# Optimization experiments

Measured on AMD Instinct MI355X. Metric: run time of the kernel, lower is better.

Reference implementation:

```python
import jax, jax.numpy as jnp
import numpy as np

B, T, V, H, E = 64, 64, 32000, 512, 256
EPS = 0.1
CLAMP_MIN = 1e-8


def setup_inputs() -> dict:
    key = jax.random.key(0)
    ks = jax.random.split(key, 7)
    s = 0.05  # small init scale to keep logits in a sane range
    return {
        "embedding": jax.random.normal(ks[0], (V, E), jnp.float32) * s,
        "w_ih": jax.random.normal(ks[1], (3 * H, E), jnp.float32) * s,
        "b_ih": jax.random.normal(ks[2], (3 * H,), jnp.float32) * s,
        "w_hh": jax.random.normal(ks[3], (3 * H, H), jnp.float32) * s,
        "b_hh": jax.random.normal(ks[4], (3 * H,), jnp.float32) * s,
        "w_out": jax.random.normal(ks[5], (V, H), jnp.float32) * s,
        "b_out": jax.random.normal(ks[6], (V,), jnp.float32) * s,
    }


def _gru_cell(x, h, w_ih, b_ih, w_hh, b_hh):
    # torch GRUCell: gates ordered (r, z, n)
    gi = x @ w_ih.T + b_ih          # [B, 3H]
    gh = h @ w_hh.T + b_hh          # [B, 3H]
    gi_r, gi_z, gi_n = jnp.split(gi, 3, axis=1)
    gh_r, gh_z, gh_n = jnp.split(gh, 3, axis=1)
    r = jax.nn.sigmoid(gi_r + gh_r)
    z = jax.nn.sigmoid(gi_z + gh_z)
    n = jnp.tanh(gi_n + r * gh_n)
    return (1.0 - z) * n + z * h


def reference(embedding, w_ih, b_ih, w_hh, b_hh, w_out, b_out):
    log_unif = -jnp.log(jnp.float32(V))

    def step(carry, key):
        hidden, inputs = carry
        hidden = _gru_cell(inputs, hidden, w_ih, b_ih, w_hh, b_hh)
        dist = jax.nn.log_softmax(hidden @ w_out.T + b_out, axis=-1)  # [B, V]
        dist_new = jax.lax.stop_gradient(dist)
        prob = jnp.exp(dist_new)
        prob_mean = prob.mean(0)  # [V]
        k_eps, k_gum = jax.random.split(key)
        # eps-sample: with prob EPS replace row with uniform log-prob
        draw = EPS >= jax.random.uniform(k_eps, (B,))
        dist_eps = jnp.where(draw[:, None], log_unif, dist_new)
        # Gumbel-max sampling
        u = jax.random.uniform(k_gum, (B, V), minval=1e-9, maxval=1.0)
        sampled = jnp.argmax(dist_eps - jnp.log(-jnp.log(u)), axis=1)  # [B]
        idx = sampled[:, None]
        logprob = jnp.take_along_axis(dist, idx, axis=1)[:, 0]
        onpolicy = jnp.clip(jnp.take_along_axis(prob, idx, axis=1)[:, 0], CLAMP_MIN, 1.0)
        offpolicy = jnp.clip(jnp.exp(jnp.take_along_axis(dist_eps, idx, axis=1)[:, 0]), CLAMP_MIN, 1.0)
        correction = onpolicy / offpolicy
        inputs_next = embedding[sampled]  # [B, E]
        return (hidden, inputs_next), (sampled, correction, logprob, dist, prob_mean)

    hidden0 = jnp.zeros((B, H), jnp.float32)
    inputs0 = jnp.broadcast_to(embedding[0], (B, E))  # embedding of zero token
    keys = jax.random.split(jax.random.key(1), T)
    _, (samples, corrections, logprobs, dists, probs) = jax.lax.scan(
        step, (hidden0, inputs0), keys)
    # scan stacks along time: transpose to batch-major like torch.cat(dim=1)
    return (samples.T,            # [B, T] int
            corrections.T,        # [B, T]
            logprobs.T,           # [B, T]
            dists.transpose(1, 0, 2),  # [B, T, V]
            probs)                # [T, V]
```

## Files before the change

kernel.cpp:

```cpp
#include <hip/hip_runtime.h>
#include <cstdint>
#include <cstddef>


#define JAX_PARTITIONABLE 1

#define Bn 64
#define Tn 64
#define Vn 32000
#define Hn 512
#define En 256

#define NSTRIP 500
#define SPAD   512

typedef unsigned short u16;
typedef __attribute__((ext_vector_type(8))) __bf16 bf16x8;
typedef __attribute__((ext_vector_type(4))) float f32x4;
typedef __attribute__((ext_vector_type(4))) uint32_t u32x4;

#define OUT_SAMP 0
#define OUT_CORR (Bn * Tn)
#define OUT_LOGP (2 * Bn * Tn)
#define OUT_DIST (3 * Bn * Tn)
#define OUT_PROB (3 * Bn * Tn + (size_t)Bn * Tn * Vn)

#define WS_HT0  0
#define WS_HT1  (WS_HT0 + Hn * Bn)
#define WS_RM   (WS_HT1 + Hn * Bn)
#define WS_RL   (WS_RM + Tn * Bn)
#define WS_SMP  (WS_RL + Tn * Bn)
#define WS_CNT  (WS_SMP + Bn)
#define WS_HS0  (WS_CNT + Bn)
#define WS_HS1  (WS_HS0 + Bn * Hn / 2)
#define WS_HS2  (WS_HS1 + Bn * Hn / 2)
#define WS_PM   (WS_HS2 + Bn * Hn / 2)
#define WS_PS   (WS_PM + Bn * SPAD)
#define WS_PBS  (WS_PS + Bn * SPAD)
#define WS_PBV  (WS_PBS + Bn * SPAD)
#define WS_PBZ  (WS_PBV + Bn * SPAD)

__device__ __forceinline__ void tf2x32(uint32_t k0, uint32_t k1,
                                       uint32_t x0, uint32_t x1,
                                       uint32_t& o0, uint32_t& o1) {
  uint32_t ks2 = k0 ^ k1 ^ 0x1BD11BDAu;
  x0 += k0; x1 += k1;
#define TFR(r) { x0 += x1; x1 = (x1 << r) | (x1 >> (32 - r)); x1 ^= x0; }
  TFR(13) TFR(15) TFR(26) TFR(6)  x0 += k1;  x1 += ks2 + 1u;
  TFR(17) TFR(29) TFR(16) TFR(24) x0 += ks2; x1 += k0 + 2u;
  TFR(13) TFR(15) TFR(26) TFR(6)  x0 += k0;  x1 += k1 + 3u;
  TFR(17) TFR(29) TFR(16) TFR(24) x0 += k1;  x1 += ks2 + 4u;
  TFR(13) TFR(15) TFR(26) TFR(6)  x0 += ks2; x1 += k0 + 5u;
#undef TFR
  o0 = x0; o1 = x1;
}

__device__ __forceinline__ uint32_t jax_bits32(uint32_t k0, uint32_t k1,
                                               uint32_t i, uint32_t total) {
#if JAX_PARTITIONABLE
  (void)total;
  uint32_t o0, o1; tf2x32(k0, k1, 0u, i, o0, o1); return o0 ^ o1;
#else
  uint32_t half = total >> 1;
  uint32_t o0, o1;
  if (i < half) { tf2x32(k0, k1, i, i + half, o0, o1); return o0; }
  tf2x32(k0, k1, i - half, i, o0, o1); return o1;
#endif
}

__device__ __forceinline__ void jax_splitkey(uint32_t k0, uint32_t k1,
                                             uint32_t idx, uint32_t num,
                                             uint32_t& s0, uint32_t& s1) {
#if JAX_PARTITIONABLE
  (void)num;
  tf2x32(k0, k1, 0u, idx, s0, s1);
#else
  uint32_t j0 = 2 * idx, j1 = 2 * idx + 1;
  uint32_t r0, r1;
  if (j0 < num) { tf2x32(k0, k1, j0, j0 + num, r0, r1); s0 = r0; }
  else          { tf2x32(k0, k1, j0 - num, j0, r0, r1); s0 = r1; }
  if (j1 < num) { tf2x32(k0, k1, j1, j1 + num, r0, r1); s1 = r0; }
  else          { tf2x32(k0, k1, j1 - num, j1, r0, r1); s1 = r1; }
#endif
}

__device__ __forceinline__ float bits_to_unit(uint32_t bits) {
  return __uint_as_float((bits >> 9) | 0x3F800000u) - 1.0f;
}

struct Limbs3 { uint32_t p0, p1, p2; };

__device__ __forceinline__ Limbs3 split3_pair(float xa, float xb) {
  const uint32_t a0 = __float_as_uint(xa) & 0xFFFF0000u;
  const float ar1 = xa - __uint_as_float(a0);
  const uint32_t a1 = __float_as_uint(ar1) & 0xFFFF0000u;
  const float ar2 = ar1 - __uint_as_float(a1);
  const uint32_t a2 = __float_as_uint(ar2) & 0xFFFF0000u;
  const uint32_t b0 = __float_as_uint(xb) & 0xFFFF0000u;
  const float br1 = xb - __uint_as_float(b0);
  const uint32_t b1 = __float_as_uint(br1) & 0xFFFF0000u;
  const float br2 = br1 - __uint_as_float(b1);
  const uint32_t b2 = __float_as_uint(br2) & 0xFFFF0000u;
  Limbs3 r;
  r.p0 = (a0 >> 16) | b0;
  r.p1 = (a1 >> 16) | b1;
  r.p2 = (a2 >> 16) | b2;
  return r;
}


__global__ void init_k(float* h0, int* sampled, int* cnt) {
  int i = blockIdx.x * 256 + threadIdx.x;
  if (i < Bn * Hn) h0[i] = 0.0f;
  if (i < Bn) { sampled[i] = 0; cnt[i] = 0; }
}

__global__ __launch_bounds__(256) void gru_fused(
    const float* __restrict__ emb,
    const float* __restrict__ w_ih, const float* __restrict__ b_ih,
    const float* __restrict__ w_hh, const float* __restrict__ b_hh,
    const float* __restrict__ hT_prev, float* __restrict__ hT_new,
    const int* __restrict__ sampled,
    u16* __restrict__ hs0, u16* __restrict__ hs1, u16* __restrict__ hs2) {
  const int tid = threadIdx.x;
  const int b = tid & 63;
  const int w = __builtin_amdgcn_readfirstlane(tid >> 6);
  const int q = w & 1;
  const int kh = w >> 1;
  const int j = blockIdx.x * 2 + q;

  __shared__ float Xs[En][64];
  {
    const int g = tid >> 6;
    const float* src = emb + (size_t)sampled[b] * En + g * 64;
#pragma unroll
    for (int kk = 0; kk < 64; kk += 4) {
      float4 v = *(const float4*)(src + kk);
      Xs[g * 64 + kk + 0][b] = v.x;
      Xs[g * 64 + kk + 1][b] = v.y;
      Xs[g * 64 + kk + 2][b] = v.z;
      Xs[g * 64 + kk + 3][b] = v.w;
    }
  }
  __syncthreads();

  float a_r = 0.f, a_z = 0.f, a_n = 0.f;
  float g_r = 0.f, g_z = 0.f, g_n = 0.f;

  {
    const float* wr = w_ih + (size_t)j * En;
    const float* wz = w_ih + (size_t)(Hn + j) * En;
    const float* wn = w_ih + (size_t)(2 * Hn + j) * En;
    const int kb = kh * 128;
#pragma unroll 8
    for (int k = kb; k < kb + 128; k++) {
      const float xv = Xs[k][b];
      a_r = fmaf(xv, wr[k], a_r);
      a_z = fmaf(xv, wz[k], a_z);
      a_n = fmaf(xv, wn[k], a_n);
    }
  }
  {
    const float* wr = w_hh + (size_t)j * Hn;
    const float* wz = w_hh + (size_t)(Hn + j) * Hn;
    const float* wn = w_hh + (size_t)(2 * Hn + j) * Hn;
    const int kb = kh * 256;
#pragma unroll 8
    for (int k = kb; k < kb + 256; k++) {
      const float hv = hT_prev[k * 64 + b];
      g_r = fmaf(hv, wr[k], g_r);
      g_z = fmaf(hv, wz[k], g_z);
      g_n = fmaf(hv, wn[k], g_n);
    }
  }

  __shared__ float red[6][2][64];
  if (kh == 1) {
    red[0][q][b] = a_r; red[1][q][b] = a_z; red[2][q][b] = a_n;
    red[3][q][b] = g_r; red[4][q][b] = g_z; red[5][q][b] = g_n;
  }
  __syncthreads();
  if (kh == 0) {
    a_r += red[0][q][b]; a_z += red[1][q][b]; a_n += red[2][q][b];
    g_r += red[3][q][b]; g_z += red[4][q][b]; g_n += red[5][q][b];
    const float gr = a_r + b_ih[j] + g_r + b_hh[j];
    const float gz = a_z + b_ih[Hn + j] + g_z + b_hh[Hn + j];
    const float r = 1.0f / (1.0f + expf(-gr));
    const float z = 1.0f / (1.0f + expf(-gz));
    const float ghn = g_n + b_hh[2 * Hn + j];
    const float n = tanhf(a_n + b_ih[2 * Hn + j] + r * ghn);
    const float hp = hT_prev[j * 64 + b];
    const float h = (1.0f - z) * n + z * hp;
    hT_new[j * 64 + b] = h;
    const uint32_t c0 = __float_as_uint(h) & 0xFFFF0000u;
    const float r1 = h - __uint_as_float(c0);
    const uint32_t c1 = __float_as_uint(r1) & 0xFFFF0000u;
    const float r2 = r1 - __uint_as_float(c1);
    const size_t ho = (size_t)b * Hn + j;
    hs0[ho] = (u16)(c0 >> 16);
    hs1[ho] = (u16)(c1 >> 16);
    hs2[ho] = (u16)(__float_as_uint(r2) >> 16);
  }
}

__global__ __launch_bounds__(256, 2) void logits_mfma(
    const u16* __restrict__ hs0, const u16* __restrict__ hs1,
    const u16* __restrict__ hs2,
    const float* __restrict__ w_out, const float* __restrict__ b_out,
    float* __restrict__ out_dist,
    float* __restrict__ pM, float* __restrict__ pS, float* __restrict__ pBS,
    int* __restrict__ pBV, float* __restrict__ pBZ,
    int* __restrict__ cnt, float* __restrict__ rmA, float* __restrict__ rlA,
    int* __restrict__ sampled, float* __restrict__ out, int t) {
  const int tid = threadIdx.x;
  const int w = tid >> 6;
  const int lane = tid & 63;
  const int wm = (w >> 1) * 32;
  const int wn = (w & 1) * 32;
  const int lr = lane & 15;
  const int lg = lane >> 4;
  const int v0 = blockIdx.x * 64;

  __shared__ int s_dr[64];
  __shared__ float ldsM[64][2], ldsS[64][2], ldsBS[64][2], ldsBZ[64][2];
  __shared__ int ldsBV[64][2];
  __shared__ int s_tk;

  uint32_t kt0, kt1, kg0, kg1;
  jax_splitkey(0u, 1u, (uint32_t)t, (uint32_t)Tn, kt0, kt1);
  jax_splitkey(kt0, kt1, 1u, 2u, kg0, kg1);
  if (tid < 64) {
    uint32_t ke0, ke1;
    jax_splitkey(kt0, kt1, 0u, 2u, ke0, ke1);
    const uint32_t eb = jax_bits32(ke0, ke1, (uint32_t)tid, (uint32_t)Bn);
    s_dr[tid] = (0.1f >= bits_to_unit(eb)) ? 1 : 0;
  }
  __syncthreads();

  f32x4 acc[2][2] = {};

#pragma unroll 2
  for (int k0 = 0; k0 < Hn; k0 += 32) {
    bf16x8 a0[2], a1[2], a2[2];
#pragma unroll
    for (int mi = 0; mi < 2; mi++) {
      const size_t off = (size_t)(wm + mi * 16 + lr) * Hn + k0 + lg * 8;
      a0[mi] = *reinterpret_cast<const bf16x8*>(hs0 + off);
      a1[mi] = *reinterpret_cast<const bf16x8*>(hs1 + off);
      a2[mi] = *reinterpret_cast<const bf16x8*>(hs2 + off);
    }
    bf16x8 bb0[2], bb1[2], bb2[2];
#pragma unroll
    for (int ni = 0; ni < 2; ni++) {
      const float* src = w_out + (size_t)(v0 + wn + ni * 16 + lr) * Hn + k0 + lg * 8;
      const float4 x0 = *(const float4*)(src);
      const float4 x1 = *(const float4*)(src + 4);
      u32x4 q0, q1, q2;
      const Limbs3 l0 = split3_pair(x0.x, x0.y);
      const Limbs3 l1 = split3_pair(x0.z, x0.w);
      const Limbs3 l2 = split3_pair(x1.x, x1.y);
      const Limbs3 l3 = split3_pair(x1.z, x1.w);
      q0[0] = l0.p0; q1[0] = l0.p1; q2[0] = l0.p2;
      q0[1] = l1.p0; q1[1] = l1.p1; q2[1] = l1.p2;
      q0[2] = l2.p0; q1[2] = l2.p1; q2[2] = l2.p2;
      q0[3] = l3.p0; q1[3] = l3.p1; q2[3] = l3.p2;
      bb0[ni] = __builtin_bit_cast(bf16x8, q0);
      bb1[ni] = __builtin_bit_cast(bf16x8, q1);
      bb2[ni] = __builtin_bit_cast(bf16x8, q2);
    }
#pragma unroll
    for (int mi = 0; mi < 2; mi++)
#pragma unroll
      for (int ni = 0; ni < 2; ni++) {
        f32x4 c = acc[mi][ni];
        c = __builtin_amdgcn_mfma_f32_16x16x32_bf16(a0[mi], bb0[ni], c, 0, 0, 0);
        c = __builtin_amdgcn_mfma_f32_16x16x32_bf16(a0[mi], bb1[ni], c, 0, 0, 0);
        c = __builtin_amdgcn_mfma_f32_16x16x32_bf16(a1[mi], bb0[ni], c, 0, 0, 0);
        c = __builtin_amdgcn_mfma_f32_16x16x32_bf16(a1[mi], bb1[ni], c, 0, 0, 0);
        c = __builtin_amdgcn_mfma_f32_16x16x32_bf16(a0[mi], bb2[ni], c, 0, 0, 0);
        c = __builtin_amdgcn_mfma_f32_16x16x32_bf16(a2[mi], bb0[ni], c, 0, 0, 0);
        acc[mi][ni] = c;
      }
  }

  float bias[2];
#pragma unroll
  for (int ni = 0; ni < 2; ni++) bias[ni] = b_out[v0 + wn + ni * 16 + lr];
#pragma unroll
  for (int mi = 0; mi < 2; mi++)
#pragma unroll
    for (int ni = 0; ni < 2; ni++)
#pragma unroll
      for (int r = 0; r < 4; r++) {
        acc[mi][ni][r] += bias[ni];
        const int brow = wm + mi * 16 + lg * 4 + r;
        out_dist[(size_t)(brow * Tn + t) * Vn + v0 + wn + ni * 16 + lr] =
            acc[mi][ni][r];
      }

  const float LU = -logf((float)Vn);
#pragma unroll
  for (int mi = 0; mi < 2; mi++) {
#pragma unroll
    for (int r = 0; r < 4; r++) {
      const int brow = wm + mi * 16 + lg * 4 + r;
      const int dr = s_dr[brow];
      const int vA = v0 + wn + lr, vB = vA + 16;
      const float zA = acc[mi][0][r], zB = acc[mi][1][r];
      float mz = fmaxf(zA, zB);
#pragma unroll
      for (int off = 1; off < 16; off <<= 1) mz = fmaxf(mz, __shfl_xor(mz, off, 64));
      float sz = expf(zA - mz) + expf(zB - mz);
#pragma unroll
      for (int off = 1; off < 16; off <<= 1) sz += __shfl_xor(sz, off, 64);
      const uint32_t bA = jax_bits32(kg0, kg1, (uint32_t)(brow * Vn + vA), 0u);
      const uint32_t bB = jax_bits32(kg0, kg1, (uint32_t)(brow * Vn + vB), 0u);
      const float uA = fmaxf(1e-9f, bits_to_unit(bA) + 1e-9f);
      const float uB = fmaxf(1e-9f, bits_to_unit(bB) + 1e-9f);
      const float glA = logf(-logf(uA));
      const float glB = logf(-logf(uB));
      const float sA = (dr ? LU : zA) - glA;
      const float sB = (dr ? LU : zB) - glB;
      float bs; int bv; float bz;
      if (sB > sA) { bs = sB; bv = vB; bz = zB; }
      else         { bs = sA; bv = vA; bz = zA; }
#pragma unroll
      for (int off = 1; off < 16; off <<= 1) {
        const float so = __shfl_xor(bs, off, 64);
        const int vo = __shfl_xor(bv, off, 64);
        const float zo = __shfl_xor(bz, off, 64);
        if (so > bs || (so == bs && vo < bv)) { bs = so; bv = vo; bz = zo; }
      }
      if (lr == 0) {
        ldsM[brow][w & 1] = mz; ldsS[brow][w & 1] = sz;
        ldsBS[brow][w & 1] = bs; ldsBV[brow][w & 1] = bv; ldsBZ[brow][w & 1] = bz;
      }
    }
  }
  __syncthreads();
  if (tid < 64) {
    const float m0 = ldsM[tid][0], m1 = ldsM[tid][1];
    const float mm = fmaxf(m0, m1);
    const float ss = ldsS[tid][0] * expf(m0 - mm) + ldsS[tid][1] * expf(m1 - mm);
    float bs = ldsBS[tid][0]; int bv = ldsBV[tid][0]; float bz = ldsBZ[tid][0];
    if (ldsBS[tid][1] > bs || (ldsBS[tid][1] == bs && ldsBV[tid][1] < bv)) {
      bs = ldsBS[tid][1]; bv = ldsBV[tid][1]; bz = ldsBZ[tid][1];
    }
    const int o = tid * SPAD + blockIdx.x;
    pM[o] = mm; pS[o] = ss; pBS[o] = bs; pBV[o] = bv; pBZ[o] = bz;
  }
  __syncthreads();

  if (tid == 0) {
    __threadfence();
    s_tk = __hip_atomic_fetch_add(&cnt[t], 1, __ATOMIC_ACQ_REL,
                                  __HIP_MEMORY_SCOPE_AGENT);
  }
  __syncthreads();
  const int ticket = s_tk;
  if (ticket >= NSTRIP - 8 && ticket < NSTRIP) {
    while (__hip_atomic_load(&cnt[t], __ATOMIC_ACQUIRE,
                             __HIP_MEMORY_SCOPE_AGENT) < NSTRIP) {
      __builtin_amdgcn_s_sleep(8);
    }
    const int base = (ticket - (NSTRIP - 8)) * 8;
    const int g = tid >> 5, l32 = tid & 31;
    const int row = base + g;
    float m = -INFINITY, ssum = 0.f;
    float bs = -INFINITY; int bv = Vn; float bz = 0.f;
    for (int s = l32; s < NSTRIP; s += 32) {
      const int o = row * SPAD + s;
      const float m2 = pM[o], s2 = pS[o];
      const float mn = fmaxf(m, m2);
      ssum = ssum * expf(m - mn) + s2 * expf(m2 - mn);
      m = mn;
      const float b2 = pBS[o]; const int v2 = pBV[o];
      if (b2 > bs || (b2 == bs && v2 < bv)) { bs = b2; bv = v2; bz = pBZ[o]; }
    }
#pragma unroll
    for (int off = 16; off >= 1; off >>= 1) {
      const float mo = __shfl_xor(m, off, 64);
      const float so = __shfl_xor(ssum, off, 64);
      const float mn = fmaxf(m, mo);
      ssum = ssum * expf(m - mn) + so * expf(mo - mn);
      m = mn;
      const float bo = __shfl_xor(bs, off, 64);
      const int vo = __shfl_xor(bv, off, 64);
      const float zo = __shfl_xor(bz, off, 64);
      if (bo > bs || (bo == bs && vo < bv)) { bs = bo; bv = vo; bz = zo; }
    }
    if (l32 == 0) {
      const float l = logf(ssum);
      rmA[t * Bn + row] = m;
      rlA[t * Bn + row] = l;
      sampled[row] = bv;
      out[OUT_SAMP + row * Tn + t] = (float)bv;
      const float d = (bz - m) - l;
      out[OUT_LOGP + row * Tn + t] = d;
      uint32_t ke0, ke1;
      jax_splitkey(kt0, kt1, 0u, 2u, ke0, ke1);
      const int dr =
          (0.1f >= bits_to_unit(jax_bits32(ke0, ke1, (uint32_t)row, (uint32_t)Bn)))
              ? 1 : 0;
      const float onp = fminf(fmaxf(expf(d), 1e-8f), 1.0f);
      const float offp = fminf(fmaxf(expf(dr ? LU : d), 1e-8f), 1.0f);
      out[OUT_CORR + row * Tn + t] = onp / offp;
    }
  }
}

__global__ void norm_all_k(float* __restrict__ out_dist,
                           float* __restrict__ probs,
                           const float* __restrict__ rmA,
                           const float* __restrict__ rlA) {
  const int blk = blockIdx.x;
  const int t = blk / 250;
  const int c = blk % 250;
  const int tid = threadIdx.x;
  const int v = c * 128 + (tid & 127);
  const int half = tid >> 7;
  __shared__ float sm[64], sl[64];
  if (tid < 64) { sm[tid] = rmA[t * Bn + tid]; sl[tid] = rlA[t * Bn + tid]; }
  __syncthreads();
  float s = 0.f;
  for (int i = 0; i < 32; i++) {
    const int b = half * 32 + i;
    float* p = out_dist + (size_t)(b * Tn + t) * Vn + v;
    const float d = (*p - sm[b]) - sl[b];
    *p = d;
    s += expf(d);
  }
  __shared__ float red[256];
  red[tid] = s; __syncthreads();
  if (half == 0)
    probs[(size_t)t * Vn + v] = (red[tid] + red[tid + 128]) * 0.015625f;
}

extern "C" void kernel_launch(void* const* d_in, const int* in_sizes, int n_in,
                              void* d_out, int out_size, void* d_ws, size_t ws_size,
                              hipStream_t stream) {
  const float* emb   = (const float*)d_in[0];
  const float* w_ih  = (const float*)d_in[1];
  const float* b_ih  = (const float*)d_in[2];
  const float* w_hh  = (const float*)d_in[3];
  const float* b_hh  = (const float*)d_in[4];
  const float* w_out = (const float*)d_in[5];
  const float* b_out = (const float*)d_in[6];
  float* out = (float*)d_out;
  float* ws  = (float*)d_ws;

  float* hT[2] = { ws + WS_HT0, ws + WS_HT1 };
  float* rmA  = ws + WS_RM;
  float* rlA  = ws + WS_RL;
  int*   smp  = (int*)(ws + WS_SMP);
  int*   cnt  = (int*)(ws + WS_CNT);
  u16*   hs0  = (u16*)(ws + WS_HS0);
  u16*   hs1  = (u16*)(ws + WS_HS1);
  u16*   hs2  = (u16*)(ws + WS_HS2);
  float* pM   = ws + WS_PM;
  float* pS   = ws + WS_PS;
  float* pBS  = ws + WS_PBS;
  int*   pBV  = (int*)(ws + WS_PBV);
  float* pBZ  = ws + WS_PBZ;

  init_k<<<(Bn * Hn + 255) / 256, 256, 0, stream>>>(hT[0], smp, cnt);

  for (int t = 0; t < Tn; t++) {
    float* hp = hT[t & 1];
    float* hn = hT[(t + 1) & 1];
    gru_fused<<<Hn / 2, 256, 0, stream>>>(emb, w_ih, b_ih, w_hh, b_hh,
                                          hp, hn, smp, hs0, hs1, hs2);
    logits_mfma<<<NSTRIP, 256, 0, stream>>>(hs0, hs1, hs2, w_out, b_out,
                                            out + OUT_DIST, pM, pS, pBS, pBV, pBZ,
                                            cnt, rmA, rlA, smp, out, t);
  }
  norm_all_k<<<Tn * 250, 256, 0, stream>>>(out + OUT_DIST, out + OUT_PROB,
                                           rmA, rlA);
}
```

Measured before the change: 8.088 ms.

## Fuse GRU, logits and normalization into one persistent kernel with grid barriers

Replaces the per-timestep pair of kernel launches and the final normalization pass with a single persistent kernel of 250 blocks that loops over time and synchronizes through a global atomic grid barrier. The GRU cell moves onto MFMA using a 3-limb bf16 split, computed by 32 of the blocks. Logits stay in registers across the barrier, so normalized log-probs and the per-token probability mean are written once instead of being re-read and rewritten by a separate pass. This removes about 128 launches and one full pass over the large dist tensor. In exchange it depends on all 250 blocks being co-resident to avoid deadlock, pays for grid-wide barriers each step, and serializes the GRU work onto a subset of blocks.

Result: slower. 27.99 ms (+246.1%).

```diff
diff --git a/kernel.cpp b/kernel.cpp
--- a/kernel.cpp
+++ b/kernel.cpp
@@ -10,9 +10,8 @@
 #define Vn 32000
 #define Hn 512
 #define En 256
-
+#define NBLK 250
 #define NSTRIP 500
-#define SPAD   512
 
 typedef unsigned short u16;
 typedef __attribute__((ext_vector_type(8))) __bf16 bf16x8;
@@ -25,20 +24,14 @@
 #define OUT_DIST (3 * Bn * Tn)
 #define OUT_PROB (3 * Bn * Tn + (size_t)Bn * Tn * Vn)
 
-#define WS_HT0  0
-#define WS_HT1  (WS_HT0 + Hn * Bn)
-#define WS_RM   (WS_HT1 + Hn * Bn)
-#define WS_RL   (WS_RM + Tn * Bn)
-#define WS_SMP  (WS_RL + Tn * Bn)
-#define WS_CNT  (WS_SMP + Bn)
-#define WS_HS0  (WS_CNT + Bn)
-#define WS_HS1  (WS_HS0 + Bn * Hn / 2)
-#define WS_HS2  (WS_HS1 + Bn * Hn / 2)
-#define WS_PM   (WS_HS2 + Bn * Hn / 2)
-#define WS_PS   (WS_PM + Bn * SPAD)
-#define WS_PBS  (WS_PS + Bn * SPAD)
-#define WS_PBV  (WS_PBS + Bn * SPAD)
-#define WS_PBZ  (WS_PBV + Bn * SPAD)
+#define WS_HT  0
+#define WS_HS  (2 * Hn * 64)
+#define WS_PM  (WS_HS + 3 * Bn * Hn)
+#define WS_PS  (WS_PM + NSTRIP * Bn)
+#define WS_PBS (WS_PS + NSTRIP * Bn)
+#define WS_PBV (WS_PBS + NSTRIP * Bn)
+#define WS_PBZ (WS_PBV + NSTRIP * Bn)
+#define WS_BAR (WS_PBZ + NSTRIP * Bn)
 
 __device__ __forceinline__ void tf2x32(uint32_t k0, uint32_t k1,
                                        uint32_t x0, uint32_t x1,
@@ -56,32 +49,14 @@
 }
 
 __device__ __forceinline__ uint32_t jax_bits32(uint32_t k0, uint32_t k1,
-                                               uint32_t i, uint32_t total) {
-#if JAX_PARTITIONABLE
-  (void)total;
+                                               uint32_t i) {
   uint32_t o0, o1; tf2x32(k0, k1, 0u, i, o0, o1); return o0 ^ o1;
-#else
-  uint32_t half = total >> 1;
-  uint32_t o0, o1;
-  if (i < half) { tf2x32(k0, k1, i, i + half, o0, o1); return o0; }
-  tf2x32(k0, k1, i - half, i, o0, o1); return o1;
-#endif
 }
 
 __device__ __forceinline__ void jax_splitkey(uint32_t k0, uint32_t k1,
-                                             uint32_t idx, uint32_t num,
+                                             uint32_t idx,
                                              uint32_t& s0, uint32_t& s1) {
-#if JAX_PARTITIONABLE
-  (void)num;
   tf2x32(k0, k1, 0u, idx, s0, s1);
-#else
-  uint32_t j0 = 2 * idx, j1 = 2 * idx + 1;
-  uint32_t r0, r1;
-  if (j0 < num) { tf2x32(k0, k1, j0, j0 + num, r0, r1); s0 = r0; }
-  else          { tf2x32(k0, k1, j0 - num, j0, r0, r1); s0 = r1; }
-  if (j1 < num) { tf2x32(k0, k1, j1, j1 + num, r0, r1); s1 = r0; }
-  else          { tf2x32(k0, k1, j1 - num, j1, r0, r1); s1 = r1; }
-#endif
 }
 
 __device__ __forceinline__ float bits_to_unit(uint32_t bits) {
@@ -108,110 +83,67 @@
   return r;
 }
 
-
-__global__ void init_k(float* h0, int* sampled, int* cnt) {
-  int i = blockIdx.x * 256 + threadIdx.x;
-  if (i < Bn * Hn) h0[i] = 0.0f;
-  if (i < Bn) { sampled[i] = 0; cnt[i] = 0; }
-}
-
-__global__ __launch_bounds__(256) void gru_fused(
+__device__ __forceinline__ void split3_frag(const float4& x0, const float4& x1,
+                                            uint32_t msk,
+                                            bf16x8& f0, bf16x8& f1, bf16x8& f2) {
+  u32x4 q0, q1, q2;
+  const Limbs3 l0 = split3_pair(x0.x, x0.y);
+  const Limbs3 l1 = split3_pair(x0.z, x0.w);
+  const Limbs3 l2 = split3_pair(x1.x, x1.y);
+  const Limbs3 l3 = split3_pair(x1.z, x1.w);
+  q0[0] = l0.p0 & msk; q1[0] = l0.p1 & msk; q2[0] = l0.p2 & msk;
+  q0[1] = l1.p0 & msk; q1[1] = l1.p1 & msk; q2[1] = l1.p2 & msk;
+  q0[2] = l2.p0 & msk; q1[2] = l2.p1 & msk; q2[2] = l2.p2 & msk;
+  q0[3] = l3.p0 & msk; q1[3] = l3.p1 & msk; q2[3] = l3.p2 & msk;
+  f0 = __builtin_bit_cast(bf16x8, q0);
+  f1 = __builtin_bit_cast(bf16x8, q1);
+  f2 = __builtin_bit_cast(bf16x8, q2);
+}
+
+__device__ __forceinline__ f32x4 mfma6(const bf16x8& a0, const bf16x8& a1,
+                                       const bf16x8& a2, const bf16x8& b0,
+                                       const bf16x8& b1, const bf16x8& b2,
+                                       f32x4 c) {
+  c = __builtin_amdgcn_mfma_f32_16x16x32_bf16(a0, b0, c, 0, 0, 0);
+  c = __builtin_amdgcn_mfma_f32_16x16x32_bf16(a0, b1, c, 0, 0, 0);
+  c = __builtin_amdgcn_mfma_f32_16x16x32_bf16(a1, b0, c, 0, 0, 0);
+  c = __builtin_amdgcn_mfma_f32_16x16x32_bf16(a1, b1, c, 0, 0, 0);
+  c = __builtin_amdgcn_mfma_f32_16x16x32_bf16(a0, b2, c, 0, 0, 0);
+  c = __builtin_amdgcn_mfma_f32_16x16x32_bf16(a2, b0, c, 0, 0, 0);
+  return c;
+}
+
+__device__ __forceinline__ void gridbar(int* bar, int target) {
+  __syncthreads();
+  if (threadIdx.x == 0) {
+    __threadfence();
+    __hip_atomic_fetch_add(bar, 1, __ATOMIC_ACQ_REL, __HIP_MEMORY_SCOPE_AGENT);
+    while (__hip_atomic_load(bar, __ATOMIC_ACQUIRE,
+                             __HIP_MEMORY_SCOPE_AGENT) < target) {
+      __builtin_amdgcn_s_sleep(1);
+    }
+  }
+  __syncthreads();
+  __threadfence();
+}
+
+__global__ void init_k(float* hT, uint32_t* hsw, int* bar) {
+  const int i = blockIdx.x * 256 + threadIdx.x;
+  if (i < 2 * Hn * 64) hT[i] = 0.0f;
+  if (i < 3 * Bn * Hn) hsw[i] = 0u;
+  if (i == 0) *bar = 0;
+}
+
+__global__ __launch_bounds__(256, 2) void mega(
     const float* __restrict__ emb,
     const float* __restrict__ w_ih, const float* __restrict__ b_ih,
     const float* __restrict__ w_hh, const float* __restrict__ b_hh,
-    const float* __restrict__ hT_prev, float* __restrict__ hT_new,
-    const int* __restrict__ sampled,
-    u16* __restrict__ hs0, u16* __restrict__ hs1, u16* __restrict__ hs2) {
-  const int tid = threadIdx.x;
-  const int b = tid & 63;
-  const int w = __builtin_amdgcn_readfirstlane(tid >> 6);
-  const int q = w & 1;
-  const int kh = w >> 1;
-  const int j = blockIdx.x * 2 + q;
-
-  __shared__ float Xs[En][64];
-  {
-    const int g = tid >> 6;
-    const float* src = emb + (size_t)sampled[b] * En + g * 64;
-#pragma unroll
-    for (int kk = 0; kk < 64; kk += 4) {
-      float4 v = *(const float4*)(src + kk);
-      Xs[g * 64 + kk + 0][b] = v.x;
-      Xs[g * 64 + kk + 1][b] = v.y;
-      Xs[g * 64 + kk + 2][b] = v.z;
-      Xs[g * 64 + kk + 3][b] = v.w;
-    }
-  }
-  __syncthreads();
-
-  float a_r = 0.f, a_z = 0.f, a_n = 0.f;
-  float g_r = 0.f, g_z = 0.f, g_n = 0.f;
-
-  {
-    const float* wr = w_ih + (size_t)j * En;
-    const float* wz = w_ih + (size_t)(Hn + j) * En;
-    const float* wn = w_ih + (size_t)(2 * Hn + j) * En;
-    const int kb = kh * 128;
-#pragma unroll 8
-    for (int k = kb; k < kb + 128; k++) {
-      const float xv = Xs[k][b];
-      a_r = fmaf(xv, wr[k], a_r);
-      a_z = fmaf(xv, wz[k], a_z);
-      a_n = fmaf(xv, wn[k], a_n);
-    }
-  }
-  {
-    const float* wr = w_hh + (size_t)j * Hn;
-    const float* wz = w_hh + (size_t)(Hn + j) * Hn;
-    const float* wn = w_hh + (size_t)(2 * Hn + j) * Hn;
-    const int kb = kh * 256;
-#pragma unroll 8
-    for (int k = kb; k < kb + 256; k++) {
-      const float hv = hT_prev[k * 64 + b];
-      g_r = fmaf(hv, wr[k], g_r);
-      g_z = fmaf(hv, wz[k], g_z);
-      g_n = fmaf(hv, wn[k], g_n);
-    }
-  }
-
-  __shared__ float red[6][2][64];
-  if (kh == 1) {
-    red[0][q][b] = a_r; red[1][q][b] = a_z; red[2][q][b] = a_n;
-    red[3][q][b] = g_r; red[4][q][b] = g_z; red[5][q][b] = g_n;
-  }
-  __syncthreads();
-  if (kh == 0) {
-    a_r += red[0][q][b]; a_z += red[1][q][b]; a_n += red[2][q][b];
-    g_r += red[3][q][b]; g_z += red[4][q][b]; g_n += red[5][q][b];
-    const float gr = a_r + b_ih[j] + g_r + b_hh[j];
-    const float gz = a_z + b_ih[Hn + j] + g_z + b_hh[Hn + j];
-    const float r = 1.0f / (1.0f + expf(-gr));
-    const float z = 1.0f / (1.0f + expf(-gz));
-    const float ghn = g_n + b_hh[2 * Hn + j];
-    const float n = tanhf(a_n + b_ih[2 * Hn + j] + r * ghn);
-    const float hp = hT_prev[j * 64 + b];
-    const float h = (1.0f - z) * n + z * hp;
-    hT_new[j * 64 + b] = h;
-    const uint32_t c0 = __float_as_uint(h) & 0xFFFF0000u;
-    const float r1 = h - __uint_as_float(c0);
-    const uint32_t c1 = __float_as_uint(r1) & 0xFFFF0000u;
-    const float r2 = r1 - __uint_as_float(c1);
-    const size_t ho = (size_t)b * Hn + j;
-    hs0[ho] = (u16)(c0 >> 16);
-    hs1[ho] = (u16)(c1 >> 16);
-    hs2[ho] = (u16)(__float_as_uint(r2) >> 16);
-  }
-}
-
-__global__ __launch_bounds__(256, 2) void logits_mfma(
-    const u16* __restrict__ hs0, const u16* __restrict__ hs1,
-    const u16* __restrict__ hs2,
     const float* __restrict__ w_out, const float* __restrict__ b_out,
-    float* __restrict__ out_dist,
+    float* __restrict__ out,
+    float* __restrict__ hT, u16* __restrict__ hs,
     float* __restrict__ pM, float* __restrict__ pS, float* __restrict__ pBS,
-    int* __restrict__ pBV, float* __restrict__ pBZ,
-    int* __restrict__ cnt, float* __restrict__ rmA, float* __restrict__ rlA,
-    int* __restrict__ sampled, float* __restrict__ out, int t) {
+    int* __restrict__ pBV, float* __restrict__ pBZ, int* __restrict__ bar) {
+  const int blk = blockIdx.x;
   const int tid = threadIdx.x;
   const int w = tid >> 6;
   const int lane = tid & 63;
@@ -219,221 +151,337 @@
   const int wn = (w & 1) * 32;
   const int lr = lane & 15;
   const int lg = lane >> 4;
-  const int v0 = blockIdx.x * 64;
-
+  const bool isGru = (blk < 32);
+  const float LU = -logf((float)Vn);
+
+  __shared__ float s_m[64], s_l[64];
+  __shared__ int s_smp[64];
   __shared__ int s_dr[64];
   __shared__ float ldsM[64][2], ldsS[64][2], ldsBS[64][2], ldsBZ[64][2];
   __shared__ int ldsBV[64][2];
-  __shared__ int s_tk;
-
-  uint32_t kt0, kt1, kg0, kg1;
-  jax_splitkey(0u, 1u, (uint32_t)t, (uint32_t)Tn, kt0, kt1);
-  jax_splitkey(kt0, kt1, 1u, 2u, kg0, kg1);
-  if (tid < 64) {
-    uint32_t ke0, ke1;
-    jax_splitkey(kt0, kt1, 0u, 2u, ke0, ke1);
-    const uint32_t eb = jax_bits32(ke0, ke1, (uint32_t)tid, (uint32_t)Bn);
-    s_dr[tid] = (0.1f >= bits_to_unit(eb)) ? 1 : 0;
-  }
+  __shared__ float Gs[64][66];
+  __shared__ float pc[2][64];
+
+  if (tid < 64) s_smp[tid] = 0;
   __syncthreads();
 
-  f32x4 acc[2][2] = {};
-
-#pragma unroll 2
-  for (int k0 = 0; k0 < Hn; k0 += 32) {
-    bf16x8 a0[2], a1[2], a2[2];
-#pragma unroll
-    for (int mi = 0; mi < 2; mi++) {
-      const size_t off = (size_t)(wm + mi * 16 + lr) * Hn + k0 + lg * 8;
-      a0[mi] = *reinterpret_cast<const bf16x8*>(hs0 + off);
-      a1[mi] = *reinterpret_cast<const bf16x8*>(hs1 + off);
-      a2[mi] = *reinterpret_cast<const bf16x8*>(hs2 + off);
-    }
-    bf16x8 bb0[2], bb1[2], bb2[2];
+  const float* gruIh[2];
+  const float* gruHh[2];
+  float gruBias[2];
+  uint32_t gruMih[2], gruMhh[2];
+  if (isGru) {
 #pragma unroll
     for (int ni = 0; ni < 2; ni++) {
-      const float* src = w_out + (size_t)(v0 + wn + ni * 16 + lr) * Hn + k0 + lg * 8;
-      const float4 x0 = *(const float4*)(src);
-      const float4 x1 = *(const float4*)(src + 4);
-      u32x4 q0, q1, q2;
-      const Limbs3 l0 = split3_pair(x0.x, x0.y);
-      const Limbs3 l1 = split3_pair(x0.z, x0.w);
-      const Limbs3 l2 = split3_pair(x1.x, x1.y);
-      const Limbs3 l3 = split3_pair(x1.z, x1.w);
-      q0[0] = l0.p0; q1[0] = l0.p1; q2[0] = l0.p2;
-      q0[1] = l1.p0; q1[1] = l1.p1; q2[1] = l1.p2;
-      q0[2] = l2.p0; q1[2] = l2.p1; q2[2] = l2.p2;
-      q0[3] = l3.p0; q1[3] = l3.p1; q2[3] = l3.p2;
-      bb0[ni] = __builtin_bit_cast(bf16x8, q0);
-      bb1[ni] = __builtin_bit_cast(bf16x8, q1);
-      bb2[ni] = __builtin_bit_cast(bf16x8, q2);
-    }
-#pragma unroll
-    for (int mi = 0; mi < 2; mi++)
-#pragma unroll
-      for (int ni = 0; ni < 2; ni++) {
-        f32x4 c = acc[mi][ni];
-        c = __builtin_amdgcn_mfma_f32_16x16x32_bf16(a0[mi], bb0[ni], c, 0, 0, 0);
-        c = __builtin_amdgcn_mfma_f32_16x16x32_bf16(a0[mi], bb1[ni], c, 0, 0, 0);
-        c = __builtin_amdgcn_mfma_f32_16x16x32_bf16(a1[mi], bb0[ni], c, 0, 0, 0);
-        c = __builtin_amdgcn_mfma_f32_16x16x32_bf16(a1[mi], bb1[ni], c, 0, 0, 0);
-        c = __builtin_amdgcn_mfma_f32_16x16x32_bf16(a0[mi], bb2[ni], c, 0, 0, 0);
-        c = __builtin_amdgcn_mfma_f32_16x16x32_bf16(a2[mi], bb0[ni], c, 0, 0, 0);
-        acc[mi][ni] = c;
-      }
-  }
-
-  float bias[2];
-#pragma unroll
-  for (int ni = 0; ni < 2; ni++) bias[ni] = b_out[v0 + wn + ni * 16 + lr];
-#pragma unroll
-  for (int mi = 0; mi < 2; mi++)
-#pragma unroll
-    for (int ni = 0; ni < 2; ni++)
-#pragma unroll
-      for (int r = 0; r < 4; r++) {
-        acc[mi][ni][r] += bias[ni];
-        const int brow = wm + mi * 16 + lg * 4 + r;
-        out_dist[(size_t)(brow * Tn + t) * Vn + v0 + wn + ni * 16 + lr] =
-            acc[mi][ni][r];
-      }
-
-  const float LU = -logf((float)Vn);
-#pragma unroll
-  for (int mi = 0; mi < 2; mi++) {
-#pragma unroll
-    for (int r = 0; r < 4; r++) {
-      const int brow = wm + mi * 16 + lg * 4 + r;
-      const int dr = s_dr[brow];
-      const int vA = v0 + wn + lr, vB = vA + 16;
-      const float zA = acc[mi][0][r], zB = acc[mi][1][r];
-      float mz = fmaxf(zA, zB);
-#pragma unroll
-      for (int off = 1; off < 16; off <<= 1) mz = fmaxf(mz, __shfl_xor(mz, off, 64));
-      float sz = expf(zA - mz) + expf(zB - mz);
-#pragma unroll
-      for (int off = 1; off < 16; off <<= 1) sz += __shfl_xor(sz, off, 64);
-      const uint32_t bA = jax_bits32(kg0, kg1, (uint32_t)(brow * Vn + vA), 0u);
-      const uint32_t bB = jax_bits32(kg0, kg1, (uint32_t)(brow * Vn + vB), 0u);
-      const float uA = fmaxf(1e-9f, bits_to_unit(bA) + 1e-9f);
-      const float uB = fmaxf(1e-9f, bits_to_unit(bB) + 1e-9f);
-      const float glA = logf(-logf(uA));
-      const float glB = logf(-logf(uB));
-      const float sA = (dr ? LU : zA) - glA;
-      const float sB = (dr ? LU : zB) - glB;
-      float bs; int bv; float bz;
-      if (sB > sA) { bs = sB; bv = vB; bz = zB; }
-      else         { bs = sA; bv = vA; bz = zA; }
-#pragma unroll
-      for (int off = 1; off < 16; off <<= 1) {
-        const float so = __shfl_xor(bs, off, 64);
-        const int vo = __shfl_xor(bv, off, 64);
-        const float zo = __shfl_xor(bz, off, 64);
-        if (so > bs || (so == bs && vo < bv)) { bs = so; bv = vo; bz = zo; }
-      }
-      if (lr == 0) {
-        ldsM[brow][w & 1] = mz; ldsS[brow][w & 1] = sz;
-        ldsBS[brow][w & 1] = bs; ldsBV[brow][w & 1] = bv; ldsBZ[brow][w & 1] = bz;
-      }
+      const int C = blk * 64 + wn + ni * 16 + lr;
+      const int gate = C & 3, j = C >> 2;
+      int ihRow = j, hhRow = j;
+      uint32_t mih = 0xFFFFFFFFu, mhh = 0xFFFFFFFFu;
+      float bias;
+      if (gate == 0)      { bias = b_ih[j] + b_hh[j]; }
+      else if (gate == 1) { ihRow = 512 + j; hhRow = 512 + j;
+                            bias = b_ih[512 + j] + b_hh[512 + j]; }
+      else if (gate == 2) { ihRow = 1024 + j; hhRow = 0; mhh = 0u;
+                            bias = b_ih[1024 + j]; }
+      else                { ihRow = 0; mih = 0u; hhRow = 1024 + j;
+                            bias = b_hh[1024 + j]; }
+      gruIh[ni] = w_ih + (size_t)ihRow * En;
+      gruHh[ni] = w_hh + (size_t)hhRow * Hn;
+      gruMih[ni] = mih; gruMhh[ni] = mhh; gruBias[ni] = bias;
     }
   }
-  __syncthreads();
-  if (tid < 64) {
-    const float m0 = ldsM[tid][0], m1 = ldsM[tid][1];
-    const float mm = fmaxf(m0, m1);
-    const float ss = ldsS[tid][0] * expf(m0 - mm) + ldsS[tid][1] * expf(m1 - mm);
-    float bs = ldsBS[tid][0]; int bv = ldsBV[tid][0]; float bz = ldsBZ[tid][0];
-    if (ldsBS[tid][1] > bs || (ldsBS[tid][1] == bs && ldsBV[tid][1] < bv)) {
-      bs = ldsBS[tid][1]; bv = ldsBV[tid][1]; bz = ldsBZ[tid][1];
+
+  int syncno = 0;
+
+  for (int t = 0; t < Tn; t++) {
+    const u16* hsPrev = hs + (size_t)((t + 1) & 1) * (3 * Bn * Hn);
+    u16* hsCur = hs + (size_t)(t & 1) * (3 * Bn * Hn);
+    const float* hTprev = hT + (size_t)((t + 1) & 1) * (Hn * 64);
+    float* hTcur = hT + (size_t)(t & 1) * (Hn * 64);
+
+    if (isGru) {
+      f32x4 gacc[2][2] = {};
+      for (int k0 = 0; k0 < En + Hn; k0 += 32) {
+        bf16x8 a0[2], a1[2], a2[2];
+        if (k0 < En) {
+#pragma unroll
+          for (int mi = 0; mi < 2; mi++) {
+            const int b = wm + mi * 16 + lr;
+            const float* sp = emb + (size_t)s_smp[b] * En + k0 + lg * 8;
+            const float4 x0 = *(const float4*)sp;
+            const float4 x1 = *(const float4*)(sp + 4);
+            split3_frag(x0, x1, 0xFFFFFFFFu, a0[mi], a1[mi], a2[mi]);
+          }
+        } else {
+#pragma unroll
+          for (int mi = 0; mi < 2; mi++) {
+            const int b = wm + mi * 16 + lr;
+            const u16* hp = hsPrev + (size_t)b * Hn + (k0 - En) + lg * 8;
+            a0[mi] = *(const bf16x8*)(hp);
+            a1[mi] = *(const bf16x8*)(hp + Bn * Hn);
+            a2[mi] = *(const bf16x8*)(hp + 2 * Bn * Hn);
+          }
+        }
+        bf16x8 b0f[2], b1f[2], b2f[2];
+#pragma unroll
+        for (int ni = 0; ni < 2; ni++) {
+          const float* sp;
+          uint32_t msk;
+          if (k0 < En) { sp = gruIh[ni] + k0 + lg * 8; msk = gruMih[ni]; }
+          else         { sp = gruHh[ni] + (k0 - En) + lg * 8; msk = gruMhh[ni]; }
+          const float4 x0 = *(const float4*)sp;
+          const float4 x1 = *(const float4*)(sp + 4);
+          split3_frag(x0, x1, msk, b0f[ni], b1f[ni], b2f[ni]);
+        }
+#pragma unroll
+        for (int mi = 0; mi < 2; mi++)
+#pragma unroll
+          for (int ni = 0; ni < 2; ni++)
+            gacc[mi][ni] = mfma6(a0[mi], a1[mi], a2[mi],
+                                 b0f[ni], b1f[ni], b2f[ni], gacc[mi][ni]);
+      }
+#pragma unroll
+      for (int mi = 0; mi < 2; mi++)
+#pragma unroll
+        for (int ni = 0; ni < 2; ni++)
+#pragma unroll
+          for (int r = 0; r < 4; r++)
+            Gs[wn + ni * 16 + lr][wm + mi * 16 + lg * 4 + r] =
+                gacc[mi][ni][r] + gruBias[ni];
+      __syncthreads();
+#pragma unroll
+      for (int u = 0; u < 4; u++) {
+        const int p = tid + u * 256;
+        const int jp = p >> 6, b = p & 63;
+        const int jg = blk * 16 + jp;
+        const float gr = Gs[4 * jp + 0][b], gz = Gs[4 * jp + 1][b];
+        const float gin = Gs[4 * jp + 2][b], ghn = Gs[4 * jp + 3][b];
+        const float rr = 1.0f / (1.0f + expf(-gr));
+        const float zz = 1.0f / (1.0f + expf(-gz));
+        const float nn = tanhf(gin + rr * ghn);
+        const float hp = hTprev[jg * 64 + b];
+        const float h = (1.0f - zz) * nn + zz * hp;
+        hTcur[jg * 64 + b] = h;
+        const uint32_t c0 = __float_as_uint(h) & 0xFFFF0000u;
+        const float r1 = h - __uint_as_float(c0);
+        const uint32_t c1 = __float_as_uint(r1) & 0xFFFF0000u;
+        const float r2 = r1 - __uint_as_float(c1);
+        const size_t ho = (size_t)b * Hn + jg;
+        hsCur[ho] = (u16)(c0 >> 16);
+        hsCur[Bn * Hn + ho] = (u16)(c1 >> 16);
+        hsCur[2 * Bn * Hn + ho] = (u16)(__float_as_uint(r2) >> 16);
+      }
     }
-    const int o = tid * SPAD + blockIdx.x;
-    pM[o] = mm; pS[o] = ss; pBS[o] = bs; pBV[o] = bv; pBZ[o] = bz;
+    gridbar(bar, (++syncno) * NBLK);
+
+    uint32_t kt0, kt1, kg0, kg1;
+    jax_splitkey(0u, 1u, (uint32_t)t, kt0, kt1);
+    jax_splitkey(kt0, kt1, 1u, kg0, kg1);
+    if (tid < 64) {
+      uint32_t ke0, ke1;
+      jax_splitkey(kt0, kt1, 0u, ke0, ke1);
+      const uint32_t eb = jax_bits32(ke0, ke1, (uint32_t)tid);
+      s_dr[tid] = (0.1f >= bits_to_unit(eb)) ? 1 : 0;
+    }
+    __syncthreads();
+
+    f32x4 acc0[2][2] = {};
+    f32x4 acc1[2][2] = {};
+    const int v0a = (2 * blk) * 64;
+    const int v0b = v0a + 64;
+
+    for (int k0 = 0; k0 < Hn; k0 += 32) {
+      bf16x8 a0[2], a1[2], a2[2];
+#pragma unroll
+      for (int mi = 0; mi < 2; mi++) {
+        const u16* hp = hsCur + (size_t)(wm + mi * 16 + lr) * Hn + k0 + lg * 8;
+        a0[mi] = *(const bf16x8*)(hp);
+        a1[mi] = *(const bf16x8*)(hp + Bn * Hn);
+        a2[mi] = *(const bf16x8*)(hp + 2 * Bn * Hn);
+      }
+      bf16x8 s0b0[2], s0b1[2], s0b2[2], s1b0[2], s1b1[2], s1b2[2];
+#pragma unroll
+      for (int ni = 0; ni < 2; ni++) {
+        const float* sp = w_out + (size_t)(v0a + wn + ni * 16 + lr) * Hn + k0 + lg * 8;
+        const float4 x0 = *(const float4*)sp;
+        const float4 x1 = *(const float4*)(sp + 4);
+        split3_frag(x0, x1, 0xFFFFFFFFu, s0b0[ni], s0b1[ni], s0b2[ni]);
+      }
+#pragma unroll
+      for (int ni = 0; ni < 2; ni++) {
+        const float* sp = w_out + (size_t)(v0b + wn + ni * 16 + lr) * Hn + k0 + lg * 8;
+        const float4 x0 = *(const float4*)sp;
+        const float4 x1 = *(const float4*)(sp + 4);
+        split3_frag(x0, x1, 0xFFFFFFFFu, s1b0[ni], s1b1[ni], s1b2[ni]);
+      }
+#pragma unroll
+      for (int mi = 0; mi < 2; mi++)
+#pragma unroll
+        for (int ni = 0; ni < 2; ni++) {
+          acc0[mi][ni] = mfma6(a0[mi], a1[mi], a2[mi],
+                               s0b0[ni], s0b1[ni], s0b2[ni], acc0[mi][ni]);
+          acc1[mi][ni] = mfma6(a0[mi], a1[mi], a2[mi],
+                               s1b0[ni], s1b1[ni], s1b2[ni], acc1[mi][ni]);
+        }
+    }
+
+    auto publish = [&](f32x4 (&acc)[2][2], const int strip, const int v0) {
+      float bias[2];
+#pragma unroll
+      for (int ni = 0; ni < 2; ni++) bias[ni] = b_out[v0 + wn + ni * 16 + lr];
+#pragma unroll
+      for (int mi = 0; mi < 2; mi++)
+#pragma unroll
+        for (int ni = 0; ni < 2; ni++)
+#pragma unroll
+          for (int r = 0; r < 4; r++) acc[mi][ni][r] += bias[ni];
+
+#pragma unroll
+      for (int mi = 0; mi < 2; mi++) {
+#pragma unroll
+        for (int r = 0; r < 4; r++) {
+          const int brow = wm + mi * 16 + lg * 4 + r;
+          const int dr = s_dr[brow];
+          const int vA = v0 + wn + lr, vB = vA + 16;
+          const float zA = acc[mi][0][r], zB = acc[mi][1][r];
+          float mz = fmaxf(zA, zB);
+#pragma unroll
+          for (int off = 1; off < 16; off <<= 1)
+            mz = fmaxf(mz, __shfl_xor(mz, off, 64));
+          float sz = expf(zA - mz) + expf(zB - mz);
+#pragma unroll
+          for (int off = 1; off < 16; off <<= 1) sz += __shfl_xor(sz, off, 64);
+          const uint32_t bA = jax_bits32(kg0, kg1, (uint32_t)(brow * Vn + vA));
+          const uint32_t bB = jax_bits32(kg0, kg1, (uint32_t)(brow * Vn + vB));
+          const float uA = fmaxf(1e-9f, bits_to_unit(bA) + 1e-9f);
+          const float uB = fmaxf(1e-9f, bits_to_unit(bB) + 1e-9f);
+          const float glA = logf(-logf(uA));
+          const float glB = logf(-logf(uB));
+          const float sA = (dr ? LU : zA) - glA;
+          const float sB = (dr ? LU : zB) - glB;
+          float bs; int bv; float bz;
+          if (sB > sA) { bs = sB; bv = vB; bz = zB; }
+          else         { bs = sA; bv = vA; bz = zA; }
+#pragma unroll
+          for (int off = 1; off < 16; off <<= 1) {
+            const float so = __shfl_xor(bs, off, 64);
+            const int vo = __shfl_xor(bv, off, 64);
+            const float zo = __shfl_xor(bz, off, 64);
+            if (so > bs || (so == bs && vo < bv)) { bs = so; bv = vo; bz = zo; }
+          }
+          if (lr == 0) {
+            ldsM[brow][w & 1] = mz; ldsS[brow][w & 1] = sz;
+            ldsBS[brow][w & 1] = bs; ldsBV[brow][w & 1] = bv;
+            ldsBZ[brow][w & 1] = bz;
+          }
+        }
+      }
+      __syncthreads();
+      if (tid < 64) {
+        const float m0 = ldsM[tid][0], m1 = ldsM[tid][1];
+        const float mm = fmaxf(m0, m1);
+        const float ss = ldsS[tid][0] * expf(m0 - mm) + ldsS[tid][1] * expf(m1 - mm);
+        float bs = ldsBS[tid][0]; int bv = ldsBV[tid][0]; float bz = ldsBZ[tid][0];
+        if (ldsBS[tid][1] > bs || (ldsBS[tid][1] == bs && ldsBV[tid][1] < bv)) {
+          bs = ldsBS[tid][1]; bv = ldsBV[tid][1]; bz = ldsBZ[tid][1];
+        }
+        const int o = strip * 64 + tid;
+        pM[o] = mm; pS[o] = ss; pBS[o] = bs; pBV[o] = bv; pBZ[o] = bz;
+      }
+      __syncthreads();
+    };
+    publish(acc0, 2 * blk, v0a);
+    publish(acc1, 2 * blk + 1, v0b);
+
+    gridbar(bar, (++syncno) * NBLK);
+
+    {
+      const int row = tid >> 2, q = tid & 3;
+      float m = -INFINITY, S = 0.f;
+      for (int i = 0; i < NSTRIP / 4; i++) {
+        const int s = q * (NSTRIP / 4) + i;
+        const float m2 = pM[s * 64 + row], s2 = pS[s * 64 + row];
+        const float mn = fmaxf(m, m2);
+        S = S * expf(m - mn) + s2 * expf(m2 - mn);
+        m = mn;
+      }
+#pragma unroll
+      for (int off = 1; off <= 2; off <<= 1) {
+        const float mo = __shfl_xor(m, off, 64);
+        const float so = __shfl_xor(S, off, 64);
+        const float mn = fmaxf(m, mo);
+        S = S * expf(m - mn) + so * expf(mo - mn);
+        m = mn;
+      }
+      const float l = logf(S);
+      if (q == 0) { s_m[row] = m; s_l[row] = l; }
+
+      if (isGru) {
+        float bs = -INFINITY; int bv = Vn; float bz = 0.f;
+        for (int i = 0; i < NSTRIP / 4; i++) {
+          const int s = q * (NSTRIP / 4) + i;
+          const int o = s * 64 + row;
+          const float b2 = pBS[o]; const int v2 = pBV[o];
+          if (b2 > bs || (b2 == bs && v2 < bv)) {
+            bs = b2; bv = v2;
+            if (blk == 0) bz = pBZ[o];
+          }
+        }
+#pragma unroll
+        for (int off = 1; off <= 2; off <<= 1) {
+          const float bo = __shfl_xor(bs, off, 64);
+          const int vo = __shfl_xor(bv, off, 64);
+          const float zo = __shfl_xor(bz, off, 64);
+          if (bo > bs || (bo == bs && vo < bv)) { bs = bo; bv = vo; bz = zo; }
+        }
+        if (q == 0) {
+          s_smp[row] = bv;
+          if (blk == 0) {
+            out[OUT_SAMP + row * Tn + t] = (float)bv;
+            const float d = (bz - m) - l;
+            out[OUT_LOGP + row * Tn + t] = d;
+            const float onp = fminf(fmaxf(expf(d), 1e-8f), 1.0f);
+            const float offp =
+                fminf(fmaxf(expf(s_dr[row] ? LU : d), 1e-8f), 1.0f);
+            out[OUT_CORR + row * Tn + t] = onp / offp;
+          }
+        }
+      }
+    }
+    __syncthreads();
+
+    auto finalize = [&](f32x4 (&acc)[2][2], const int v0) {
+      float ce0 = 0.f, ce1 = 0.f;
+#pragma unroll
+      for (int mi = 0; mi < 2; mi++)
+#pragma unroll
+        for (int r = 0; r < 4; r++) {
+          const int brow = wm + mi * 16 + lg * 4 + r;
+          const float m = s_m[brow], l = s_l[brow];
+          const float d0 = (acc[mi][0][r] - m) - l;
+          const float d1 = (acc[mi][1][r] - m) - l;
+          out[OUT_DIST + (size_t)(brow * Tn + t) * Vn + v0 + wn + lr] = d0;
+          out[OUT_DIST + (size_t)(brow * Tn + t) * Vn + v0 + wn + 16 + lr] = d1;
+          ce0 += expf(d0);
+          ce1 += expf(d1);
+        }
+#pragma unroll
+      for (int off = 16; off <= 32; off <<= 1) {
+        ce0 += __shfl_xor(ce0, off, 64);
+        ce1 += __shfl_xor(ce1, off, 64);
+      }
+      if (lg == 0) {
+        pc[w >> 1][wn + lr] = ce0;
+        pc[w >> 1][wn + 16 + lr] = ce1;
+      }
+      __syncthreads();
+      if (tid < 64)
+        out[OUT_PROB + (size_t)t * Vn + v0 + tid] =
+            (pc[0][tid] + pc[1][tid]) * 0.015625f;
+      __syncthreads();
+    };
+    finalize(acc0, v0a);
+    finalize(acc1, v0b);
   }
-  __syncthreads();
-
-  if (tid == 0) {
-    __threadfence();
-    s_tk = __hip_atomic_fetch_add(&cnt[t], 1, __ATOMIC_ACQ_REL,
-                                  __HIP_MEMORY_SCOPE_AGENT);
-  }
-  __syncthreads();
-  const int ticket = s_tk;
-  if (ticket >= NSTRIP - 8 && ticket < NSTRIP) {
-    while (__hip_atomic_load(&cnt[t], __ATOMIC_ACQUIRE,
-                             __HIP_MEMORY_SCOPE_AGENT) < NSTRIP) {
-      __builtin_amdgcn_s_sleep(8);
-    }
-    const int base = (ticket - (NSTRIP - 8)) * 8;
-    const int g = tid >> 5, l32 = tid & 31;
-    const int row = base + g;
-    float m = -INFINITY, ssum = 0.f;
-    float bs = -INFINITY; int bv = Vn; float bz = 0.f;
-    for (int s = l32; s < NSTRIP; s += 32) {
-      const int o = row * SPAD + s;
-      const float m2 = pM[o], s2 = pS[o];
-      const float mn = fmaxf(m, m2);
-      ssum = ssum * expf(m - mn) + s2 * expf(m2 - mn);
-      m = mn;
-      const float b2 = pBS[o]; const int v2 = pBV[o];
-      if (b2 > bs || (b2 == bs && v2 < bv)) { bs = b2; bv = v2; bz = pBZ[o]; }
-    }
-#pragma unroll
-    for (int off = 16; off >= 1; off >>= 1) {
-      const float mo = __shfl_xor(m, off, 64);
-      const float so = __shfl_xor(ssum, off, 64);
-      const float mn = fmaxf(m, mo);
-      ssum = ssum * expf(m - mn) + so * expf(mo - mn);
-      m = mn;
-      const float bo = __shfl_xor(bs, off, 64);
-      const int vo = __shfl_xor(bv, off, 64);
-      const float zo = __shfl_xor(bz, off, 64);
-      if (bo > bs || (bo == bs && vo < bv)) { bs = bo; bv = vo; bz = zo; }
-    }
-    if (l32 == 0) {
-      const float l = logf(ssum);
-      rmA[t * Bn + row] = m;
-      rlA[t * Bn + row] = l;
-      sampled[row] = bv;
-      out[OUT_SAMP + row * Tn + t] = (float)bv;
-      const float d = (bz - m) - l;
-      out[OUT_LOGP + row * Tn + t] = d;
-      uint32_t ke0, ke1;
-      jax_splitkey(kt0, kt1, 0u, 2u, ke0, ke1);
-      const int dr =
-          (0.1f >= bits_to_unit(jax_bits32(ke0, ke1, (uint32_t)row, (uint32_t)Bn)))
-              ? 1 : 0;
-      const float onp = fminf(fmaxf(expf(d), 1e-8f), 1.0f);
-      const float offp = fminf(fmaxf(expf(dr ? LU : d), 1e-8f), 1.0f);
-      out[OUT_CORR + row * Tn + t] = onp / offp;
-    }
-  }
-}
-
-__global__ void norm_all_k(float* __restrict__ out_dist,
-                           float* __restrict__ probs,
-                           const float* __restrict__ rmA,
-                           const float* __restrict__ rlA) {
-  const int blk = blockIdx.x;
-  const int t = blk / 250;
-  const int c = blk % 250;
-  const int tid = threadIdx.x;
-  const int v = c * 128 + (tid & 127);
-  const int half = tid >> 7;
-  __shared__ float sm[64], sl[64];
-  if (tid < 64) { sm[tid] = rmA[t * Bn + tid]; sl[tid] = rlA[t * Bn + tid]; }
-  __syncthreads();
-  float s = 0.f;
-  for (int i = 0; i < 32; i++) {
-    const int b = half * 32 + i;
-    float* p = out_dist + (size_t)(b * Tn + t) * Vn + v;
-    const float d = (*p - sm[b]) - sl[b];
-    *p = d;
-    s += expf(d);
-  }
-  __shared__ float red[256];
-  red[tid] = s; __syncthreads();
-  if (half == 0)
-    probs[(size_t)t * Vn + v] = (red[tid] + red[tid + 128]) * 0.015625f;
 }
 
 extern "C" void kernel_launch(void* const* d_in, const int* in_sizes, int n_in,
@@ -449,31 +497,16 @@
   float* out = (float*)d_out;
   float* ws  = (float*)d_ws;
 
-  float* hT[2] = { ws + WS_HT0, ws + WS_HT1 };
-  float* rmA  = ws + WS_RM;
-  float* rlA  = ws + WS_RL;
-  int*   smp  = (int*)(ws + WS_SMP);
-  int*   cnt  = (int*)(ws + WS_CNT);
-  u16*   hs0  = (u16*)(ws + WS_HS0);
-  u16*   hs1  = (u16*)(ws + WS_HS1);
-  u16*   hs2  = (u16*)(ws + WS_HS2);
-  float* pM   = ws + WS_PM;
-  float* pS   = ws + WS_PS;
-  float* pBS  = ws + WS_PBS;
-  int*   pBV  = (int*)(ws + WS_PBV);
-  float* pBZ  = ws + WS_PBZ;
-
-  init_k<<<(Bn * Hn + 255) / 256, 256, 0, stream>>>(hT[0], smp, cnt);
-
-  for (int t = 0; t < Tn; t++) {
-    float* hp = hT[t & 1];
-    float* hn = hT[(t + 1) & 1];
-    gru_fused<<<Hn / 2, 256, 0, stream>>>(emb, w_ih, b_ih, w_hh, b_hh,
-                                          hp, hn, smp, hs0, hs1, hs2);
-    logits_mfma<<<NSTRIP, 256, 0, stream>>>(hs0, hs1, hs2, w_out, b_out,
-                                            out + OUT_DIST, pM, pS, pBS, pBV, pBZ,
-                                            cnt, rmA, rlA, smp, out, t);
-  }
-  norm_all_k<<<Tn * 250, 256, 0, stream>>>(out + OUT_DIST, out + OUT_PROB,
-                                           rmA, rlA);
-}
+  float* hT  = ws + WS_HT;
+  u16*   hs  = (u16*)(ws + WS_HS);
+  float* pM  = ws + WS_PM;
+  float* pS  = ws + WS_PS;
+  float* pBS = ws + WS_PBS;
+  int*   pBV = (int*)(ws + WS_PBV);
+  float* pBZ = ws + WS_PBZ;
+  int*   bar = (int*)(ws + WS_BAR);
+
+  init_k<<<(3 * Bn * Hn + 255) / 256, 256, 0, stream>>>(hT, (uint32_t*)hs, bar);
+  mega<<<NBLK, 256, 0, stream>>>(emb, w_ih, b_ih, w_hh, b_hh, w_out, b_out,
+                                 out, hT, hs, pM, pS, pBS, pBV, pBZ, bar);
+}
```
